# Kernel tuning notes

Hardware: AMD Instinct MI355X
Metric: run time of the kernel (lower is better)

## Reference

```python
import jax, jax.numpy as jnp
import numpy as np

B, N, F = 4, 256, 128
H = 256  # hidden width of readout MLP
OUT = 1


def setup_inputs() -> dict:
    key = jax.random.key(0)
    k_x, k_wp, k_w1, k_b1, k_w2, k_b2 = jax.random.split(key, 6)
    node_embeddings = jax.random.normal(k_x, (B, N, F), dtype=jnp.float32)
    # layer_pooled: Linear(F, F, bias=False); stored as [in, out]
    W_pool = jax.random.normal(k_wp, (F, F), dtype=jnp.float32) / np.sqrt(F)
    # readout layer 1: Linear(3F, H, bias=True)
    W1 = jax.random.normal(k_w1, (3 * F, H), dtype=jnp.float32) / np.sqrt(3 * F)
    b1 = jax.random.normal(k_b1, (H,), dtype=jnp.float32) * 0.01
    # readout layer 2: Linear(H, OUT, bias=True)
    W2 = jax.random.normal(k_w2, (H, OUT), dtype=jnp.float32) / np.sqrt(H)
    b2 = jax.random.normal(k_b2, (OUT,), dtype=jnp.float32) * 0.01
    return {"node_embeddings": node_embeddings, "W_pool": W_pool,
            "W1": W1, "b1": b1, "W2": W2, "b2": b2}


def reference(node_embeddings, W_pool, W1, b1, W2, b2):
    b, n, f = node_embeddings.shape
    # pooled context: mean over nodes, then Linear(F,F) (no bias)
    h_pooled = jnp.einsum('bf,fh->bh', node_embeddings.mean(axis=1), W_pool)  # [B,F]
    # pairwise grid: features[b,i,j] = relu(concat(h_pooled[b], x[b,i], x[b,j]))
    f_pooled = jnp.broadcast_to(h_pooled[:, None, None, :], (b, n, n, f))
    f_i = jnp.broadcast_to(node_embeddings[:, :, None, :], (b, n, n, f))  # f_expanded
    f_j = jnp.broadcast_to(node_embeddings[:, None, :, :], (b, n, n, f))  # f_expanded_diff
    features = jax.nn.relu(jnp.concatenate([f_pooled, f_i, f_j], axis=-1))  # [B,N,N,3F]
    h = jax.nn.relu(jnp.einsum('bijk,kh->bijh', features, W1) + b1)  # [B,N,N,H]
    out = jnp.einsum('bijh,ho->bijo', h, W2) + b2  # [B,N,N,OUT]
    return out
```

## Files before the change

kernel.cpp:

```cpp
#include <hip/hip_runtime.h>
#include <hip/hip_bf16.h>

#define B 4
#define N 256
#define F 128
#define H 256

__global__ __launch_bounds__(256) void kAW(
    const float* __restrict__ x, const float* __restrict__ Wp,
    const float* __restrict__ W1, const float* __restrict__ b1,
    float* __restrict__ ub, float* __restrict__ A, float* __restrict__ W) {
  __shared__ float xr[4][F];
  const int blk = blockIdx.x;
  const int rg = blk >> 1;
  const int hh = blk & 1;
  const int b = rg >> 6;
  const int i0 = (rg & 63) * 4;
  const int t = threadIdx.x;
  const int h = hh * 128 + (t & 127);
  const int rh = (t >> 7) * 2;

  {
    const int idx0 = t, idx1 = t + 256;
    xr[idx0 >> 7][idx0 & 127] =
        fmaxf(x[(b * N + i0 + (idx0 >> 7)) * F + (idx0 & 127)], 0.f);
    xr[idx1 >> 7][idx1 & 127] =
        fmaxf(x[(b * N + i0 + (idx1 >> 7)) * F + (idx1 & 127)], 0.f);
  }
  __syncthreads();

  {
    float a0 = 0.f, a1 = 0.f, q0 = 0.f, q1 = 0.f;
    const float* W1i = W1 + F * H;
    const float* W1j = W1 + 2 * F * H;
#pragma unroll 8
    for (int f = 0; f < F; ++f) {
      const float wi = W1i[f * H + h];
      const float wj = W1j[f * H + h];
      const float x0 = xr[rh + 0][f];
      const float x1 = xr[rh + 1][f];
      a0 = fmaf(x0, wi, a0); a1 = fmaf(x1, wi, a1);
      q0 = fmaf(x0, wj, q0); q1 = fmaf(x1, wj, q1);
    }
    A[(b * N + i0 + rh + 0) * H + h] = a0;
    A[(b * N + i0 + rh + 1) * H + h] = a1;
    W[(b * N + i0 + rh + 0) * H + h] = q0;
    W[(b * N + i0 + rh + 1) * H + h] = q1;
  }

  if (blk < B) {
    __shared__ float4 red4[256];
    __shared__ float xm_s[F];
    __shared__ float rp_s[F];
    __shared__ float part[256];
    const int pb = blk;
    const float4* xb4 = (const float4*)(x + pb * N * F);
    float4 acc = make_float4(0.f, 0.f, 0.f, 0.f);
#pragma unroll 8
    for (int k = 0; k < 32; ++k) {
      const float4 v = xb4[t + 256 * k];
      acc.x += v.x; acc.y += v.y; acc.z += v.z; acc.w += v.w;
    }
    red4[t] = acc;
    __syncthreads();
    if (t < 32) {
      float4 s = red4[t];
#pragma unroll
      for (int m = 1; m < 8; ++m) {
        const float4 v = red4[t + 32 * m];
        s.x += v.x; s.y += v.y; s.z += v.z; s.w += v.w;
      }
      const float inv = 1.f / (float)N;
      xm_s[4 * t + 0] = s.x * inv;
      xm_s[4 * t + 1] = s.y * inv;
      xm_s[4 * t + 2] = s.z * inv;
      xm_s[4 * t + 3] = s.w * inv;
    }
    __syncthreads();
    {
      const int lo = t & 127, kh = t >> 7;
      float p = 0.f;
      const int k0 = kh * 64;
#pragma unroll 8
      for (int kk = 0; kk < 64; ++kk) {
        const int k = k0 + kk;
        p = fmaf(xm_s[k], Wp[k * F + lo], p);
      }
      part[t] = p;
    }
    __syncthreads();
    if (t < 128) rp_s[t] = fmaxf(part[t] + part[t + 128], 0.f);
    __syncthreads();
    {
      float u = b1[t];
#pragma unroll 8
      for (int k = 0; k < F; ++k) u = fmaf(rp_s[k], W1[k * H + t], u);
      ub[pb * H + t] = u;
    }
  }
}

#define SA 34
__global__ __launch_bounds__(512) void kPair(
    const float* __restrict__ A, const float* __restrict__ W,
    const float* __restrict__ ub, const float* __restrict__ W2,
    const float* __restrict__ b2, float* __restrict__ out) {
  __shared__ float aT[256 * SA];
  __shared__ float wT[256 * SA];
  __shared__ float w2s[H];

  const int b = blockIdx.z;
  const int i0 = blockIdx.y * 32;
  const int j0 = blockIdx.x * 32;
  const int t = threadIdx.x;
  const int hh = t & 255;
  const int rh = (t >> 8) * 16;

  if (t < H) w2s[t] = W2[t];
  const float ubv = ub[b * H + hh];
  const float* Ab = A + (b * N + i0) * H;
  const float* Wb = W + (b * N + j0) * H;
#pragma unroll 8
  for (int k = 0; k < 16; ++k) {
    const int r = rh + k;
    aT[hh * SA + r] = Ab[r * H + hh] + ubv;
    wT[hh * SA + r] = Wb[r * H + hh];
  }
  __syncthreads();

  const int tj = t & 31;
  const int ti = t >> 5;
  float acc0 = 0.f, acc1 = 0.f;
  const float* ap = aT + 2 * ti;
  const float* wp = wT + tj;
#pragma unroll 4
  for (int h4 = 0; h4 < 256; h4 += 4) {
    const float4 w2v = *(const float4*)(w2s + h4);
#pragma unroll
    for (int k = 0; k < 4; ++k) {
      const int h = h4 + k;
      const float2 av = *(const float2*)(ap + h * SA);
      const float wv = wp[h * SA];
      const float w2h = (k == 0) ? w2v.x : (k == 1) ? w2v.y
                       : (k == 2) ? w2v.z : w2v.w;
      acc0 = fmaf(fmaxf(av.x + wv, 0.f), w2h, acc0);
      acc1 = fmaf(fmaxf(av.y + wv, 0.f), w2h, acc1);
    }
  }

  const float bb = b2[0];
  const int i = i0 + 2 * ti;
  const int j = j0 + tj;
  float* o = out + (b * N + i) * N + j;
  o[0] = acc0 + bb;
  o[N] = acc1 + bb;
}

extern "C" void kernel_launch(void* const* d_in, const int* in_sizes, int n_in,
                              void* d_out, int out_size, void* d_ws, size_t ws_size,
                              hipStream_t stream) {
  const float* x  = (const float*)d_in[0];
  const float* Wp = (const float*)d_in[1];
  const float* W1 = (const float*)d_in[2];
  const float* b1 = (const float*)d_in[3];
  const float* W2 = (const float*)d_in[4];
  const float* b2 = (const float*)d_in[5];
  float* out = (float*)d_out;

  float* ws = (float*)d_ws;
  float* ub = ws;
  float* A  = ub + B * H;
  float* W  = A + B * N * H;

  kAW<<<dim3(512), dim3(256), 0, stream>>>(x, Wp, W1, b1, ub, A, W);
  kPair<<<dim3(N / 32, N / 32, B), dim3(512), 0, stream>>>(A, W, ub, W2, b2, out);
}
```

Baseline: 94.67 us.

## Use packed fp16 intermediates and fdot2 for pairwise readout with register tiling

Stores the per-node projections A, W and the pooled bias as packed half2 instead of fp32. The pair kernel then computes relu(a+w) with packed fp16 adds and max, and accumulates against W2 using fdot2. Each thread now holds a 4x4 i/j tile over a 1/8 slice of H, and a shared-memory reduction combines the slices. The goal is to cut VALU instruction count and LDS traffic per output, at the cost of reduced precision in the hidden activations and an extra reduction step. The first kernel is also reshaped to 512 threads that each compute two adjacent h columns for one row.

```diff
diff --git a/kernel.cpp b/kernel.cpp
--- a/kernel.cpp
+++ b/kernel.cpp
@@ -6,59 +6,69 @@
 #define F 128
 #define H 256
 
-__global__ __launch_bounds__(256) void kAW(
+typedef _Float16 h2_t __attribute__((ext_vector_type(2)));
+static __device__ __forceinline__ unsigned int h2u(h2_t v) {
+  return __builtin_bit_cast(unsigned int, v);
+}
+static __device__ __forceinline__ h2_t uh2(unsigned int v) {
+  return __builtin_bit_cast(h2_t, v);
+}
+
+__global__ __launch_bounds__(512) void kAW(
     const float* __restrict__ x, const float* __restrict__ Wp,
     const float* __restrict__ W1, const float* __restrict__ b1,
-    float* __restrict__ ub, float* __restrict__ A, float* __restrict__ W) {
-  __shared__ float xr[4][F];
+    unsigned int* __restrict__ ubh, unsigned int* __restrict__ Ah,
+    unsigned int* __restrict__ Wh) {
+  __shared__ float xr[8][F];
   const int blk = blockIdx.x;
   const int rg = blk >> 1;
   const int hh = blk & 1;
-  const int b = rg >> 6;
-  const int i0 = (rg & 63) * 4;
+  const int b = rg >> 5;
+  const int i0 = (rg & 31) * 8;
   const int t = threadIdx.x;
-  const int h = hh * 128 + (t & 127);
-  const int rh = (t >> 7) * 2;
+  const int h2l = t & 63;
+  const int r = t >> 6;
+  const int h2g = hh * 64 + h2l;
 
   {
-    const int idx0 = t, idx1 = t + 256;
-    xr[idx0 >> 7][idx0 & 127] =
-        fmaxf(x[(b * N + i0 + (idx0 >> 7)) * F + (idx0 & 127)], 0.f);
-    xr[idx1 >> 7][idx1 & 127] =
-        fmaxf(x[(b * N + i0 + (idx1 >> 7)) * F + (idx1 & 127)], 0.f);
+    int idx = t;
+    xr[idx >> 7][idx & 127] =
+        fmaxf(x[(b * N + i0 + (idx >> 7)) * F + (idx & 127)], 0.f);
+    idx = t + 512;
+    xr[idx >> 7][idx & 127] =
+        fmaxf(x[(b * N + i0 + (idx >> 7)) * F + (idx & 127)], 0.f);
   }
   __syncthreads();
 
   {
     float a0 = 0.f, a1 = 0.f, q0 = 0.f, q1 = 0.f;
-    const float* W1i = W1 + F * H;
-    const float* W1j = W1 + 2 * F * H;
+    const float* W1i = W1 + F * H + 2 * h2g;
+    const float* W1j = W1 + 2 * F * H + 2 * h2g;
 #pragma unroll 8
     for (int f = 0; f < F; ++f) {
-      const float wi = W1i[f * H + h];
-      const float wj = W1j[f * H + h];
-      const float x0 = xr[rh + 0][f];
-      const float x1 = xr[rh + 1][f];
-      a0 = fmaf(x0, wi, a0); a1 = fmaf(x1, wi, a1);
-      q0 = fmaf(x0, wj, q0); q1 = fmaf(x1, wj, q1);
-    }
-    A[(b * N + i0 + rh + 0) * H + h] = a0;
-    A[(b * N + i0 + rh + 1) * H + h] = a1;
-    W[(b * N + i0 + rh + 0) * H + h] = q0;
-    W[(b * N + i0 + rh + 1) * H + h] = q1;
+      const float2 wi = *(const float2*)(W1i + f * H);
+      const float2 wj = *(const float2*)(W1j + f * H);
+      const float xv = xr[r][f];
+      a0 = fmaf(xv, wi.x, a0); a1 = fmaf(xv, wi.y, a1);
+      q0 = fmaf(xv, wj.x, q0); q1 = fmaf(xv, wj.y, q1);
+    }
+    h2_t av; av.x = (_Float16)a0; av.y = (_Float16)a1;
+    h2_t qv; qv.x = (_Float16)q0; qv.y = (_Float16)q1;
+    Ah[(b * N + i0 + r) * 128 + h2g] = h2u(av);
+    Wh[(b * N + i0 + r) * 128 + h2g] = h2u(qv);
   }
 
   if (blk < B) {
-    __shared__ float4 red4[256];
+    __shared__ float4 red4[512];
     __shared__ float xm_s[F];
     __shared__ float rp_s[F];
-    __shared__ float part[256];
+    __shared__ float part[512];
     const int pb = blk;
     const float4* xb4 = (const float4*)(x + pb * N * F);
     float4 acc = make_float4(0.f, 0.f, 0.f, 0.f);
-#pragma unroll 8
-    for (int k = 0; k < 32; ++k) {
-      const float4 v = xb4[t + 256 * k];
+#pragma unroll
+    for (int k = 0; k < 16; ++k) {
+      const float4 v = xb4[t + 512 * k];
       acc.x += v.x; acc.y += v.y; acc.z += v.z; acc.w += v.w;
     }
     red4[t] = acc;
@@ -66,7 +76,7 @@
     if (t < 32) {
       float4 s = red4[t];
 #pragma unroll
-      for (int m = 1; m < 8; ++m) {
+      for (int m = 1; m < 16; ++m) {
         const float4 v = red4[t + 32 * m];
         s.x += v.x; s.y += v.y; s.z += v.z; s.w += v.w;
       }
@@ -80,80 +90,138 @@
     {
       const int lo = t & 127, kh = t >> 7;
       float p = 0.f;
+      const int k0 = kh * 32;
+#pragma unroll 8
+      for (int kk = 0; kk < 32; ++kk) {
+        const int k = k0 + kk;
+        p = fmaf(xm_s[k], Wp[k * F + lo], p);
+      }
+      part[t] = p;
+    }
+    __syncthreads();
+    if (t < 128)
+      rp_s[t] = fmaxf(part[t] + part[t + 128] + part[t + 256] + part[t + 384],
+                      0.f);
+    __syncthreads();
+    {
+      const int lo = t & 255, kh = t >> 8;
+      float u = 0.f;
       const int k0 = kh * 64;
 #pragma unroll 8
       for (int kk = 0; kk < 64; ++kk) {
         const int k = k0 + kk;
-        p = fmaf(xm_s[k], Wp[k * F + lo], p);
-      }
-      part[t] = p;
-    }
-    __syncthreads();
-    if (t < 128) rp_s[t] = fmaxf(part[t] + part[t + 128], 0.f);
-    __syncthreads();
-    {
-      float u = b1[t];
-#pragma unroll 8
-      for (int k = 0; k < F; ++k) u = fmaf(rp_s[k], W1[k * H + t], u);
-      ub[pb * H + t] = u;
-    }
-  }
-}
-
-#define SA 34
+        u = fmaf(rp_s[k], W1[k * H + lo], u);
+      }
+      part[t] = u;
+    }
+    __syncthreads();
+    if (t < 256) {
+      const float u = part[t] + part[t + 256] + b1[t];
+      const float un = __shfl_down(u, 1);
+      if ((t & 1) == 0) {
+        h2_t v; v.x = (_Float16)u; v.y = (_Float16)un;
+        ubh[pb * 128 + (t >> 1)] = h2u(v);
+      }
+    }
+  }
+}
+
+#define ST 36
 __global__ __launch_bounds__(512) void kPair(
-    const float* __restrict__ A, const float* __restrict__ W,
-    const float* __restrict__ ub, const float* __restrict__ W2,
+    const unsigned int* __restrict__ Ah, const unsigned int* __restrict__ Wh,
+    const unsigned int* __restrict__ ubh, const float* __restrict__ W2,
     const float* __restrict__ b2, float* __restrict__ out) {
-  __shared__ float aT[256 * SA];
-  __shared__ float wT[256 * SA];
-  __shared__ float w2s[H];
+  __shared__ __align__(16) unsigned int sbuf[2 * 128 * ST];
+  __shared__ unsigned int w2h[128];
+  unsigned int* aT = sbuf;
+  unsigned int* wT = sbuf + 128 * ST;
 
   const int b = blockIdx.z;
   const int i0 = blockIdx.y * 32;
   const int j0 = blockIdx.x * 32;
   const int t = threadIdx.x;
-  const int hh = t & 255;
-  const int rh = (t >> 8) * 16;
-
-  if (t < H) w2s[t] = W2[t];
-  const float ubv = ub[b * H + hh];
-  const float* Ab = A + (b * N + i0) * H;
-  const float* Wb = W + (b * N + j0) * H;
-#pragma unroll 8
-  for (int k = 0; k < 16; ++k) {
-    const int r = rh + k;
-    aT[hh * SA + r] = Ab[r * H + hh] + ubv;
-    wT[hh * SA + r] = Wb[r * H + hh];
-  }
-  __syncthreads();
-
-  const int tj = t & 31;
-  const int ti = t >> 5;
-  float acc0 = 0.f, acc1 = 0.f;
-  const float* ap = aT + 2 * ti;
-  const float* wp = wT + tj;
+
+  const int hh2 = t & 127;
+  const int rg2 = t >> 7;
+  if (t < 128) {
+    h2_t v; v.x = (_Float16)W2[2 * t]; v.y = (_Float16)W2[2 * t + 1];
+    w2h[t] = h2u(v);
+  }
+  const h2_t ubv = uh2(ubh[b * 128 + hh2]);
+  const unsigned int* Ap = Ah + (b * N + i0) * 128 + hh2;
+  const unsigned int* Wp_ = Wh + (b * N + j0) * 128 + hh2;
+#pragma unroll
+  for (int g = 0; g < 2; ++g) {
+    const int rb = rg2 * 8 + g * 4;
+    const h2_t x0 = uh2(Ap[(rb + 0) * 128]) + ubv;
+    const h2_t x1 = uh2(Ap[(rb + 1) * 128]) + ubv;
+    const h2_t x2 = uh2(Ap[(rb + 2) * 128]) + ubv;
+    const h2_t x3 = uh2(Ap[(rb + 3) * 128]) + ubv;
+    uint4 av; av.x = h2u(x0); av.y = h2u(x1); av.z = h2u(x2); av.w = h2u(x3);
+    uint4 wv; wv.x = Wp_[(rb + 0) * 128]; wv.y = Wp_[(rb + 1) * 128];
+    wv.z = Wp_[(rb + 2) * 128]; wv.w = Wp_[(rb + 3) * 128];
+    *(uint4*)(aT + hh2 * ST + rb) = av;
+    *(uint4*)(wT + hh2 * ST + rb) = wv;
+  }
+  __syncthreads();
+
+  const int hs = t >> 6;
+  const int pos = t & 63;
+  const int qi = pos & 7;
+  const int qj = pos >> 3;
+  float acc[16];
+#pragma unroll
+  for (int k = 0; k < 16; ++k) acc[k] = 0.f;
+  const unsigned int* ap = aT + 4 * qi;
+  const unsigned int* wp = wT + 4 * qj;
+  const h2_t hz = {(_Float16)0.f, (_Float16)0.f};
+  const int h2a = hs * 16;
 #pragma unroll 4
-  for (int h4 = 0; h4 < 256; h4 += 4) {
-    const float4 w2v = *(const float4*)(w2s + h4);
-#pragma unroll
-    for (int k = 0; k < 4; ++k) {
-      const int h = h4 + k;
-      const float2 av = *(const float2*)(ap + h * SA);
-      const float wv = wp[h * SA];
-      const float w2h = (k == 0) ? w2v.x : (k == 1) ? w2v.y
-                       : (k == 2) ? w2v.z : w2v.w;
-      acc0 = fmaf(fmaxf(av.x + wv, 0.f), w2h, acc0);
-      acc1 = fmaf(fmaxf(av.y + wv, 0.f), w2h, acc1);
-    }
-  }
+  for (int h2i = h2a; h2i < h2a + 16; ++h2i) {
+    const uint4 a4 = *(const uint4*)(ap + h2i * ST);
+    const uint4 w4 = *(const uint4*)(wp + h2i * ST);
+    const h2_t w2v = uh2(w2h[h2i]);
+    const h2_t aa0 = uh2(a4.x), aa1 = uh2(a4.y), aa2 = uh2(a4.z),
+               aa3 = uh2(a4.w);
+    const h2_t ww0 = uh2(w4.x), ww1 = uh2(w4.y), ww2 = uh2(w4.z),
+               ww3 = uh2(w4.w);
+#pragma unroll
+    for (int si = 0; si < 4; ++si) {
+      const h2_t av = (si == 0) ? aa0 : (si == 1) ? aa1 : (si == 2) ? aa2
+                                                                    : aa3;
+#pragma unroll
+      for (int sj = 0; sj < 4; ++sj) {
+        const h2_t wv = (sj == 0) ? ww0 : (sj == 1) ? ww1 : (sj == 2) ? ww2
+                                                                      : ww3;
+        h2_t s = av + wv;
+        s = __builtin_elementwise_max(s, hz);
+        acc[si * 4 + sj] =
+            __builtin_amdgcn_fdot2(s, w2v, acc[si * 4 + sj], false);
+      }
+    }
+  }
+  __syncthreads();
+
+  float* part = (float*)sbuf;
+#pragma unroll
+  for (int k = 0; k < 16; ++k) part[t * 17 + k] = acc[k];
+  __syncthreads();
 
   const float bb = b2[0];
-  const int i = i0 + 2 * ti;
-  const int j = j0 + tj;
-  float* o = out + (b * N + i) * N + j;
-  o[0] = acc0 + bb;
-  o[N] = acc1 + bb;
+  const int oid = 2 * t;
+  const int pos2 = oid >> 4;
+  const int kk = oid & 15;
+  float s0 = 0.f, s1 = 0.f;
+#pragma unroll
+  for (int hsx = 0; hsx < 8; ++hsx) {
+    const int base = (hsx * 64 + pos2) * 17;
+    s0 += part[base + kk];
+    s1 += part[base + kk + 1];
+  }
+  const int i = 4 * (pos2 & 7) + (kk >> 2);
+  const int j = 4 * (pos2 >> 3) + (kk & 3);
+  float2 o; o.x = s0 + bb; o.y = s1 + bb;
+  *(float2*)(out + (b * N + i0 + i) * N + j0 + j) = o;
 }
 
 extern "C" void kernel_launch(void* const* d_in, const int* in_sizes, int n_in,
@@ -167,11 +235,12 @@
   const float* b2 = (const float*)d_in[5];
   float* out = (float*)d_out;
 
-  float* ws = (float*)d_ws;
-  float* ub = ws;
-  float* A  = ub + B * H;
-  float* W  = A + B * N * H;
-
-  kAW<<<dim3(512), dim3(256), 0, stream>>>(x, Wp, W1, b1, ub, A, W);
-  kPair<<<dim3(N / 32, N / 32, B), dim3(512), 0, stream>>>(A, W, ub, W2, b2, out);
-}
+  unsigned int* ws = (unsigned int*)d_ws;
+  unsigned int* Ah  = ws;
+  unsigned int* Wh  = Ah + B * N * 128;
+  unsigned int* ubh = Wh + B * N * 128;
+
+  kAW<<<dim3(256), dim3(512), 0, stream>>>(x, Wp, W1, b1, ubh, Ah, Wh);
+  kPair<<<dim3(N / 32, N / 32, B), dim3(512), 0, stream>>>(Ah, Wh, ubh, W2,
+                                                           b2, out);
+}
```

Measured after the change: 90.15 us. 1.05x faster.
